# Kernel tuning notes

Hardware: AMD Instinct MI355X
Metric: run time of the kernel (lower is better)

Reference implementation:

```python
import jax, jax.numpy as jnp
import numpy as np

NH = 8  # n_heads
LN_EPS = 1e-5

def _ln(x, g, b):
    m = x.mean(-1, keepdims=True)
    v = ((x - m) ** 2).mean(-1, keepdims=True)
    return (x - m) / jnp.sqrt(v + LN_EPS) * g + b

def _l2norm(x):
    n = jnp.sqrt(jnp.sum(x * x, axis=-1, keepdims=True))
    return x / jnp.maximum(n, 1e-12)

def _block(h, inw, inb, outw, outb, g1, b1, g2, b2, w1, bb1, w2, bb2):
    B, T, D = h.shape
    hd = D // NH
    res = h
    hn = _ln(h, g1, b1)
    qkv = hn @ inw.T + inb
    q, k, v = jnp.split(qkv, 3, axis=-1)
    q = q.reshape(B, T, NH, hd)
    k = k.reshape(B, T, NH, hd)
    v = v.reshape(B, T, NH, hd)
    scores = jnp.einsum('bthd,bshd->bhts', q, k) / jnp.sqrt(jnp.asarray(hd, h.dtype))
    a = jax.nn.softmax(scores, axis=-1)
    o = jnp.einsum('bhts,bshd->bthd', a, v).reshape(B, T, D)
    h = res + o @ outw.T + outb
    f = _ln(h, g2, b2)
    f = jax.nn.gelu(f @ w1.T + bb1, approximate=False) @ w2.T + bb2
    return h + f

def setup_inputs() -> dict:
    B, T, IN, D, L, NS, NP = 8, 1024, 1024, 512, 4, 1024, 512
    key = jax.random.key(0)
    ks = jax.random.split(key, 24)
    gn = jax.random.normal
    u = jax.random.uniform(ks[1], (B, T, NS), dtype=jnp.float32, minval=1e-6, maxval=1.0 - 1e-6)
    gumbel = -jnp.log(-jnp.log(u))
    s = lambda fan: 1.0 / np.sqrt(fan)
    inp = {
        'x': gn(ks[0], (B, T, IN), dtype=jnp.float32),
        'gumbel': gumbel,
        'sym_w': gn(ks[2], (D, IN)) * s(IN),
        'sym_b': jnp.zeros((D,)),
        'codebook': gn(ks[3], (NS, D)) * 0.1,
        'pos_enc': gn(ks[4], (1, 2000, D)) * 0.02,
        'attn_in_w': gn(ks[5], (L, 3 * D, D)) * s(D),
        'attn_in_b': jnp.zeros((L, 3 * D)),
        'attn_out_w': gn(ks[6], (L, D, D)) * s(D),
        'attn_out_b': jnp.zeros((L, D)),
        'n1_g': jnp.ones((L, D)), 'n1_b': jnp.zeros((L, D)),
        'n2_g': jnp.ones((L, D)), 'n2_b': jnp.zeros((L, D)),
        'ffn_w1': gn(ks[7], (L, 4 * D, D)) * s(D),
        'ffn_b1': jnp.zeros((L, 4 * D)),
        'ffn_w2': gn(ks[8], (L, D, 4 * D)) * s(4 * D),
        'ffn_b2': jnp.zeros((L, D)),
        'q_w': gn(ks[9], (D, D)) * s(D),
        'q_b': jnp.zeros((D,)),
        'qln_g': jnp.ones((D,)), 'qln_b': jnp.zeros((D,)),
        'patterns': gn(ks[10], (NP, D)) * s(D),
        'epoch': 0,
        'total_epochs': 100,
    }
    return inp

def reference(x, gumbel, sym_w, sym_b, codebook, pos_enc,
              attn_in_w, attn_in_b, attn_out_w, attn_out_b,
              n1_g, n1_b, n2_g, n2_b, ffn_w1, ffn_b1, ffn_w2, ffn_b2,
              q_w, q_b, qln_g, qln_b, patterns, epoch, total_epochs):
    B, T, _ = x.shape
    # SymbolizationLayer (soft, gumbel-softmax with tau=0.5)
    hp = x @ sym_w.T + sym_b                               # [B,T,D]
    logits_s = _l2norm(hp) @ _l2norm(codebook).T / 0.5     # [B,T,NS]
    soft = jax.nn.softmax((logits_s + gumbel) / 0.5, axis=-1)
    h = soft @ codebook + pos_enc[:, :T, :]
    # transformer blocks
    for i in range(attn_in_w.shape[0]):
        h = _block(h, attn_in_w[i], attn_in_b[i], attn_out_w[i], attn_out_b[i],
                   n1_g[i], n1_b[i], n2_g[i], n2_b[i],
                   ffn_w1[i], ffn_b1[i], ffn_w2[i], ffn_b2[i])
    # VQPatternMatrix (eval mode: hard assignments, no EMA updates)
    Q = _l2norm(_ln(h @ q_w.T + q_b, qln_g, qln_b))
    temp = max(0.5, 1.0 - 0.5 * epoch / total_epochs)
    logits = Q @ _l2norm(patterns).T / temp                # [B,T,NP]
    hard_idx = jnp.argmax(logits, axis=-1)                 # [B,T]
    assign = jax.nn.one_hot(hard_idx, patterns.shape[0], dtype=logits.dtype)
    emb = jnp.take(patterns, hard_idx, axis=0)             # gather = one_hot @ patterns
    return (emb, assign, logits, h, hard_idx)
```

## Files before the change

### kernel.cpp

```cpp
#include <hip/hip_runtime.h>

#define DEV __device__ __forceinline__

typedef unsigned short u16;
typedef unsigned int u32;
typedef __attribute__((ext_vector_type(8))) _Float16 h8_t;
typedef __attribute__((ext_vector_type(4))) float f4_t;

constexpr int T_SEQ = 1024;
constexpr int DMODEL = 512;
constexpr int NPAT = 512;

enum {
  E_BIAS = 0,
  E_VQ = 5,
  E_RES = 6,
  E_POS = 8,
  E_GUM2 = 9,
  E_GELU2 = 10,
  E_QKV2 = 11
};

DEV float h2f(u16 h) { return (float)__builtin_bit_cast(_Float16, h); }
DEV void split2(float x, u16& h, u16& l) {
  _Float16 hh = (_Float16)x;
  float r = x - (float)hh;
  _Float16 ll = (_Float16)r;
  h = __builtin_bit_cast(u16, hh);
  l = __builtin_bit_cast(u16, ll);
}

DEV f4_t mfh(h8_t a, h8_t b, f4_t c) {
  return __builtin_amdgcn_mfma_f32_16x16x32_f16(a, b, c, 0, 0, 0);
}
DEV f4_t prod3(h8_t ah, h8_t al, h8_t bh, h8_t bl, f4_t c) {
  c = mfh(ah, bh, c);
  c = mfh(ah, bl, c);
  c = mfh(al, bh, c);
  return c;
}

typedef const __attribute__((address_space(1))) unsigned char* gas_t;
typedef __attribute__((address_space(3))) unsigned char* las_t;
DEV void gload16(const u16* g, u16* l) {
  __builtin_amdgcn_global_load_lds((gas_t)(const void*)g, (las_t)(void*)l, 16,
                                   0, 0);
}

template <int BM, int EPI>
__global__ __launch_bounds__(256, BM == 64 ? 3 : 2) void gemm_mf(
    const u16* __restrict__ Ah, const u16* __restrict__ Al,
    const u16* __restrict__ Bh, const u16* __restrict__ Bl,
    const float* __restrict__ bias, const float* __restrict__ res,
    float* __restrict__ Cf, u16* __restrict__ Ch, u16* __restrict__ Cl, int N,
    int KK, int lda, int ldb, int gx, const int* __restrict__ ep,
    const int* __restrict__ tot) {
  constexpr int MT = BM / 32;
  constexpr int CPP = BM / 16;
  __shared__ __align__(16) u16 AsH[2][BM][4][8], AsL[2][BM][4][8];
  __shared__ __align__(16) u16 BsH[2][128][4][8], BsL[2][128][4][8];
  const int tid = threadIdx.x;
  const int w = tid >> 6, lane = tid & 63;
  const int wy = w >> 1, wx = w & 1;
  const int lr = lane & 15, lg = lane >> 4;

  const int nwg = gridDim.x;
  const int bid = blockIdx.x;
  const int qq = nwg >> 3;
  const int wg = (bid & 7) * qq + (bid >> 3);
  const int by = wg / gx, bx = wg % gx;
  const int bm = by * BM, bn = bx * 128;

  const int rowl = lane >> 2, slot4 = lane & 3;

  auto STAGE = [&](int k0, int buf) {
#pragma unroll
    for (int it = 0; it < CPP / 2; ++it) {
      const int f = w + 4 * it;
      const int plane = f / CPP;
      const int ch = f % CPP;
      const int row = ch * 16 + rowl;
      const int kp = slot4 ^ ((row >> 1) & 3);
      const size_t g = (size_t)(bm + row) * lda + k0 + kp * 8;
      if (plane == 0)
        gload16(&Ah[g], &AsH[buf][0][0][0] + ch * 512);
      else
        gload16(&Al[g], &AsL[buf][0][0][0] + ch * 512);
    }
#pragma unroll
    for (int it = 0; it < 4; ++it) {
      const int f = w + 4 * it;
      const int plane = f >> 3;
      const int ch = f & 7;
      const int row = ch * 16 + rowl;
      const int kp = slot4 ^ ((row >> 1) & 3);
      const size_t g = (size_t)(bn + row) * ldb + k0 + kp * 8;
      if (plane == 0)
        gload16(&Bh[g], &BsH[buf][0][0][0] + ch * 512);
      else
        gload16(&Bl[g], &BsL[buf][0][0][0] + ch * 512);
    }
  };

  f4_t acc[MT][4];
#pragma unroll
  for (int mt = 0; mt < MT; ++mt)
#pragma unroll
    for (int nt = 0; nt < 4; ++nt) acc[mt][nt] = (f4_t){0.f, 0.f, 0.f, 0.f};

  const int nsteps = KK / 32;
  STAGE(0, 0);
  __syncthreads();
  for (int t = 0; t < nsteps; ++t) {
    const int cur = t & 1;
    if (t + 1 < nsteps) STAGE((t + 1) * 32, cur ^ 1);

    h8_t fah[MT], fal[MT], fbh[4], fbl[4];
#pragma unroll
    for (int mt = 0; mt < MT; ++mt) {
      int row = wy * (BM / 2) + mt * 16 + lr;
      int slot = lg ^ ((row >> 1) & 3);
      fah[mt] = *(const h8_t*)&AsH[cur][row][slot][0];
      fal[mt] = *(const h8_t*)&AsL[cur][row][slot][0];
    }
#pragma unroll
    for (int nt = 0; nt < 4; ++nt) {
      int col = wx * 64 + nt * 16 + lr;
      int slot = lg ^ ((col >> 1) & 3);
      fbh[nt] = *(const h8_t*)&BsH[cur][col][slot][0];
      fbl[nt] = *(const h8_t*)&BsL[cur][col][slot][0];
    }
#pragma unroll
    for (int mt = 0; mt < MT; ++mt)
#pragma unroll
      for (int nt = 0; nt < 4; ++nt)
        acc[mt][nt] = prod3(fah[mt], fal[mt], fbh[nt], fbl[nt], acc[mt][nt]);
    __syncthreads();
  }

  float bv[4];
  if constexpr (EPI == E_BIAS || EPI == E_RES || EPI == E_GELU2 ||
                EPI == E_QKV2) {
#pragma unroll
    for (int nt = 0; nt < 4; ++nt) bv[nt] = bias[bn + wx * 64 + nt * 16 + lr];
  }
  float invt = 1.0f;
  if constexpr (EPI == E_VQ) {
    float tt = 1.0f - 0.5f * (float)ep[0] / (float)tot[0];
    invt = 1.0f / fmaxf(0.5f, tt);
  }
#pragma unroll
  for (int mt = 0; mt < MT; ++mt)
#pragma unroll
    for (int nt = 0; nt < 4; ++nt) {
      const int c = bn + wx * 64 + nt * 16 + lr;
#pragma unroll
      for (int i = 0; i < 4; ++i) {
        const int m = bm + wy * (BM / 2) + mt * 16 + 4 * lg + i;
        const size_t idx = (size_t)m * N + c;
        float v = acc[mt][nt][i];
        if constexpr (EPI == E_BIAS) {
          Cf[idx] = v + bv[nt];
        } else if constexpr (EPI == E_VQ) {
          Cf[idx] = v * invt;
        } else if constexpr (EPI == E_RES) {
          Cf[idx] = v + bv[nt] + res[idx];
        } else if constexpr (EPI == E_POS) {
          Cf[idx] = v + res[(size_t)(m & 1023) * N + c];
        } else if constexpr (EPI == E_GUM2) {
          float t = 4.0f * v + 2.0f * res[idx];
          u16 h2, l2;
          split2(t, h2, l2);
          Ch[idx] = h2;
          Cl[idx] = l2;
        } else if constexpr (EPI == E_GELU2) {
          float t = v + bv[nt];
          float g = 0.5f * t * (1.0f + erff(t * 0.7071067811865476f));
          u16 h2, l2;
          split2(g, h2, l2);
          Ch[idx] = h2;
          Cl[idx] = l2;
        } else if constexpr (EPI == E_QKV2) {
          float t = v + bv[nt];
          u16 h2, l2;
          split2(t, h2, l2);
          size_t o;
          if (c < 512) {
            o = (size_t)m * 512 + c;
          } else if (c < 1024) {
            o = 4194304 + (size_t)m * 512 + (c - 512);
          } else {
            int cc = c - 1024, hh2 = cc >> 6, dd = cc & 63;
            int bb2 = m >> 10, tt2 = m & 1023;
            o = 8388608 +
                (((size_t)(bb2 * 8 + hh2) * 64 + dd) << 10) + tt2;
          }
          Ch[o] = h2;
          Cl[o] = l2;
        }
      }
    }
}

__global__ __launch_bounds__(256, 4) void flash_mfma(
    const u16* __restrict__ QKVh, const u16* __restrict__ QKVl,
    u16* __restrict__ Oh, u16* __restrict__ Ol) {
  __shared__ __align__(16) u16 KP[2][64][8][8];
  __shared__ __align__(16) u16 Vs[2][64][8][8];
  const int tid = threadIdx.x;
  const int w = tid >> 6, lane = tid & 63;
  const int lr = lane & 15, lg = lane >> 4;
  const int bid = blockIdx.x;
  const int b = bid & 7;
  const int slot_b = bid >> 3;
  const int hh = slot_b >> 4;
  const int qt = slot_b & 15;

  const u16* Qh = QKVh;
  const u16* Ql = QKVl;
  const u16* Kh = QKVh + 4194304;
  const u16* Kl = QKVl + 4194304;
  const u16* Vh = QKVh + 8388608;
  const u16* Vl = QKVl + 8388608;

  h8_t qf[2][2];
  {
    size_t g =
        ((size_t)(b * 1024 + qt * 64 + w * 16 + lr)) * 512 + hh * 64 + lg * 8;
    qf[0][0] = *(const h8_t*)&Qh[g];
    qf[0][1] = *(const h8_t*)&Ql[g];
    qf[1][0] = *(const h8_t*)&Qh[g + 32];
    qf[1][1] = *(const h8_t*)&Ql[g + 32];
  }

  f4_t oacc[4];
#pragma unroll
  for (int nt = 0; nt < 4; ++nt) oacc[nt] = (f4_t){0.f, 0.f, 0.f, 0.f};
  float mrun[4], lrun[4];
#pragma unroll
  for (int i = 0; i < 4; ++i) {
    mrun[i] = -__builtin_huge_valf();
    lrun[i] = 0.0f;
  }

  const int rowl8 = lane >> 3, slot8 = lane & 7;

  for (int kt = 0; kt < 16; ++kt) {
    __syncthreads();
#pragma unroll
    for (int it = 0; it < 4; ++it) {
      const int f = w + 4 * it;
      const int plane = f >> 3, ch = f & 7;
      const int row = ch * 8 + rowl8;
      const int kp = slot8 ^ (row & 7);
      const size_t gk =
          ((size_t)(b * 1024 + kt * 64 + row)) * 512 + hh * 64 + kp * 8;
      if (plane == 0)
        gload16(&Kh[gk], &KP[0][0][0][0] + ch * 512);
      else
        gload16(&Kl[gk], &KP[1][0][0][0] + ch * 512);
    }
#pragma unroll
    for (int it = 0; it < 4; ++it) {
      const int f = w + 4 * it;
      const int plane = f >> 3, ch = f & 7;
      const int row = ch * 8 + rowl8;
      const int kp = slot8 ^ (row & 7);
      const size_t gv =
          ((size_t)((b * 8 + hh) * 64 + row)) * 1024 + kt * 64 + kp * 8;
      if (plane == 0)
        gload16(&Vh[gv], &Vs[0][0][0][0] + ch * 512);
      else
        gload16(&Vl[gv], &Vs[1][0][0][0] + ch * 512);
    }
    __syncthreads();

    f4_t s[4];
#pragma unroll
    for (int nt = 0; nt < 4; ++nt) {
      s[nt] = (f4_t){0.f, 0.f, 0.f, 0.f};
      const int col = nt * 16 + lr;
#pragma unroll
      for (int ks = 0; ks < 2; ++ks) {
        int slt = (ks * 4 + lg) ^ (col & 7);
        h8_t kh = *(const h8_t*)&KP[0][col][slt][0];
        h8_t kl = *(const h8_t*)&KP[1][col][slt][0];
        s[nt] = prod3(qf[ks][0], qf[ks][1], kh, kl, s[nt]);
      }
    }

#pragma unroll
    for (int i = 0; i < 4; ++i) {
      float rm = -__builtin_huge_valf();
#pragma unroll
      for (int nt = 0; nt < 4; ++nt) {
        s[nt][i] *= 0.125f;
        rm = fmaxf(rm, s[nt][i]);
      }
      rm = fmaxf(rm, __shfl_xor(rm, 1));
      rm = fmaxf(rm, __shfl_xor(rm, 2));
      rm = fmaxf(rm, __shfl_xor(rm, 4));
      rm = fmaxf(rm, __shfl_xor(rm, 8));
      float mnew = fmaxf(mrun[i], rm);
      float alpha = __expf(mrun[i] - mnew);
      float rs = 0.0f;
#pragma unroll
      for (int nt = 0; nt < 4; ++nt) {
        float p = __expf(s[nt][i] - mnew);
        s[nt][i] = p;
        rs += p;
      }
      rs += __shfl_xor(rs, 1);
      rs += __shfl_xor(rs, 2);
      rs += __shfl_xor(rs, 4);
      rs += __shfl_xor(rs, 8);
      lrun[i] = lrun[i] * alpha + rs;
      mrun[i] = mnew;
#pragma unroll
      for (int nt = 0; nt < 4; ++nt) oacc[nt][i] *= alpha;
    }

    __syncthreads();

#pragma unroll
    for (int nt = 0; nt < 4; ++nt)
#pragma unroll
      for (int i = 0; i < 4; ++i) {
        int qrow = w * 16 + 4 * lg + i;
        int kv = nt * 16 + lr;
        int kp = kv >> 3, j = kv & 7;
        int slt = kp ^ (qrow & 7);
        u16 h2, l2;
        split2(s[nt][i], h2, l2);
        KP[0][qrow][slt][j] = h2;
        KP[1][qrow][slt][j] = l2;
      }

    h8_t pf[2][2];
#pragma unroll
    for (int ks = 0; ks < 2; ++ks) {
      int row = w * 16 + lr;
      int slt = (ks * 4 + lg) ^ (row & 7);
      pf[ks][0] = *(const h8_t*)&KP[0][row][slt][0];
      pf[ks][1] = *(const h8_t*)&KP[1][row][slt][0];
    }
#pragma unroll
    for (int ntd = 0; ntd < 4; ++ntd) {
      const int col = ntd * 16 + lr;
#pragma unroll
      for (int ks = 0; ks < 2; ++ks) {
        int slt = (ks * 4 + lg) ^ (col & 7);
        h8_t vh = *(const h8_t*)&Vs[0][col][slt][0];
        h8_t vl = *(const h8_t*)&Vs[1][col][slt][0];
        oacc[ntd] = prod3(pf[ks][0], pf[ks][1], vh, vl, oacc[ntd]);
      }
    }
  }

#pragma unroll
  for (int i = 0; i < 4; ++i) {
    float inv = 1.0f / lrun[i];
    int t = qt * 64 + w * 16 + 4 * lg + i;
#pragma unroll
    for (int ntd = 0; ntd < 4; ++ntd) {
      int d = hh * 64 + ntd * 16 + lr;
      size_t idx = ((size_t)(b * 1024 + t)) * 512 + d;
      u16 h2, l2;
      split2(oacc[ntd][i] * inv, h2, l2);
      Oh[idx] = h2;
      Ol[idx] = l2;
    }
  }
}

DEV float wave_sum(float v) {
#pragma unroll
  for (int off = 1; off < 64; off <<= 1) v += __shfl_xor(v, off);
  return v;
}

DEV void store8_split2(u16* H, u16* L, size_t base, const float* t) {
  u16 vh[8], vl[8];
#pragma unroll
  for (int j = 0; j < 8; ++j) split2(t[j], vh[j], vl[j]);
  *(ushort4*)&H[base] = make_ushort4(vh[0], vh[1], vh[2], vh[3]);
  *(ushort4*)&H[base + 4] = make_ushort4(vh[4], vh[5], vh[6], vh[7]);
  *(ushort4*)&L[base] = make_ushort4(vl[0], vl[1], vl[2], vl[3]);
  *(ushort4*)&L[base + 4] = make_ushort4(vl[4], vl[5], vl[6], vl[7]);
}

__global__ __launch_bounds__(256) void ln_split2(const float* __restrict__ x,
                                                 const float* __restrict__ g,
                                                 const float* __restrict__ b,
                                                 u16* __restrict__ yh,
                                                 u16* __restrict__ yl) {
  const int row = blockIdx.x * 4 + (threadIdx.x >> 6);
  const int lane = threadIdx.x & 63;
  const float* xr = x + (size_t)row * DMODEL;
  float v[8];
  *(float4*)&v[0] = *(const float4*)(xr + lane * 8);
  *(float4*)&v[4] = *(const float4*)(xr + lane * 8 + 4);
  float s = 0.0f;
#pragma unroll
  for (int j = 0; j < 8; ++j) s += v[j];
  s = wave_sum(s);
  float mean = s * (1.0f / 512.0f);
  float s2 = 0.0f;
#pragma unroll
  for (int j = 0; j < 8; ++j) {
    float d = v[j] - mean;
    s2 += d * d;
  }
  s2 = wave_sum(s2);
  float rstd = 1.0f / sqrtf(s2 * (1.0f / 512.0f) + 1e-5f);
  float gg[8], bv[8];
  *(float4*)&gg[0] = *(const float4*)(g + lane * 8);
  *(float4*)&gg[4] = *(const float4*)(g + lane * 8 + 4);
  *(float4*)&bv[0] = *(const float4*)(b + lane * 8);
  *(float4*)&bv[4] = *(const float4*)(b + lane * 8 + 4);
  float t[8];
#pragma unroll
  for (int j = 0; j < 8; ++j) t[j] = (v[j] - mean) * rstd * gg[j] + bv[j];
  store8_split2(yh, yl, (size_t)row * DMODEL + lane * 8, t);
}

__global__ __launch_bounds__(256) void ln_l2_split2(
    const float* __restrict__ x, const float* __restrict__ g,
    const float* __restrict__ b, u16* __restrict__ yh, u16* __restrict__ yl) {
  const int row = blockIdx.x * 4 + (threadIdx.x >> 6);
  const int lane = threadIdx.x & 63;
  const float* xr = x + (size_t)row * DMODEL;
  float v[8];
  *(float4*)&v[0] = *(const float4*)(xr + lane * 8);
  *(float4*)&v[4] = *(const float4*)(xr + lane * 8 + 4);
  float s = 0.0f;
#pragma unroll
  for (int j = 0; j < 8; ++j) s += v[j];
  s = wave_sum(s);
  float mean = s * (1.0f / 512.0f);
  float s2 = 0.0f;
#pragma unroll
  for (int j = 0; j < 8; ++j) {
    float d = v[j] - mean;
    s2 += d * d;
  }
  s2 = wave_sum(s2);
  float rstd = 1.0f / sqrtf(s2 * (1.0f / 512.0f) + 1e-5f);
  float gg[8], bv[8];
  *(float4*)&gg[0] = *(const float4*)(g + lane * 8);
  *(float4*)&gg[4] = *(const float4*)(g + lane * 8 + 4);
  *(float4*)&bv[0] = *(const float4*)(b + lane * 8);
  *(float4*)&bv[4] = *(const float4*)(b + lane * 8 + 4);
  float t[8];
#pragma unroll
  for (int j = 0; j < 8; ++j) t[j] = (v[j] - mean) * rstd * gg[j] + bv[j];
  float n2 = 0.0f;
#pragma unroll
  for (int j = 0; j < 8; ++j) n2 += t[j] * t[j];
  n2 = wave_sum(n2);
  float den = fmaxf(sqrtf(n2), 1e-12f);
#pragma unroll
  for (int j = 0; j < 8; ++j) t[j] /= den;
  store8_split2(yh, yl, (size_t)row * DMODEL + lane * 8, t);
}

__global__ __launch_bounds__(256) void l2_split2(const float* __restrict__ x,
                                                 u16* __restrict__ yh,
                                                 u16* __restrict__ yl) {
  const int row = blockIdx.x * 4 + (threadIdx.x >> 6);
  const int lane = threadIdx.x & 63;
  const float* xr = x + (size_t)row * DMODEL;
  float v[8];
  *(float4*)&v[0] = *(const float4*)(xr + lane * 8);
  *(float4*)&v[4] = *(const float4*)(xr + lane * 8 + 4);
  float n2 = 0.0f;
#pragma unroll
  for (int j = 0; j < 8; ++j) n2 += v[j] * v[j];
  n2 = wave_sum(n2);
  float den = fmaxf(sqrtf(n2), 1e-12f);
#pragma unroll
  for (int j = 0; j < 8; ++j) v[j] /= den;
  store8_split2(yh, yl, (size_t)row * DMODEL + lane * 8, v);
}

__global__ __launch_bounds__(256) void softmax2(u16* __restrict__ H,
                                                u16* __restrict__ L) {
  const int row = blockIdx.x;
  const int tid = threadIdx.x;
  const size_t base = (size_t)row * 1024 + tid * 4;
  ushort4 qh = *(const ushort4*)&H[base];
  ushort4 ql = *(const ushort4*)&L[base];
  float v0 = h2f(qh.x) + h2f(ql.x);
  float v1 = h2f(qh.y) + h2f(ql.y);
  float v2 = h2f(qh.z) + h2f(ql.z);
  float v3 = h2f(qh.w) + h2f(ql.w);
  float mx = fmaxf(fmaxf(v0, v1), fmaxf(v2, v3));
#pragma unroll
  for (int off = 1; off < 64; off <<= 1) mx = fmaxf(mx, __shfl_xor(mx, off));
  __shared__ float red[4];
  const int wv = tid >> 6;
  if ((tid & 63) == 0) red[wv] = mx;
  __syncthreads();
  mx = fmaxf(fmaxf(red[0], red[1]), fmaxf(red[2], red[3]));
  float e0 = __expf(v0 - mx), e1 = __expf(v1 - mx), e2 = __expf(v2 - mx),
        e3 = __expf(v3 - mx);
  float s = e0 + e1 + e2 + e3;
#pragma unroll
  for (int off = 1; off < 64; off <<= 1) s += __shfl_xor(s, off);
  __syncthreads();
  if ((tid & 63) == 0) red[wv] = s;
  __syncthreads();
  s = red[0] + red[1] + red[2] + red[3];
  float inv = 1.0f / s;
  u16 ah[4], al[4];
  split2(e0 * inv, ah[0], al[0]);
  split2(e1 * inv, ah[1], al[1]);
  split2(e2 * inv, ah[2], al[2]);
  split2(e3 * inv, ah[3], al[3]);
  *(ushort4*)&H[base] = make_ushort4(ah[0], ah[1], ah[2], ah[3]);
  *(ushort4*)&L[base] = make_ushort4(al[0], al[1], al[2], al[3]);
}

__global__ __launch_bounds__(256) void split2_k(const float* __restrict__ src,
                                                u16* __restrict__ H,
                                                u16* __restrict__ L, int n4) {
  for (int e = blockIdx.x * 256 + threadIdx.x; e < n4; e += gridDim.x * 256) {
    float4 v = *(const float4*)(src + (size_t)e * 4);
    u16 ah[4], al[4];
    split2(v.x, ah[0], al[0]);
    split2(v.y, ah[1], al[1]);
    split2(v.z, ah[2], al[2]);
    split2(v.w, ah[3], al[3]);
    *(ushort4*)&H[(size_t)e * 4] = make_ushort4(ah[0], ah[1], ah[2], ah[3]);
    *(ushort4*)&L[(size_t)e * 4] = make_ushort4(al[0], al[1], al[2], al[3]);
  }
}

__global__ __launch_bounds__(256) void tsplit_cb(const float* __restrict__ cb,
                                                 u16* __restrict__ th,
                                                 u16* __restrict__ tl) {
  const int c = blockIdx.x;
  const int t = threadIdx.x;
  u16 ah[4], al[4];
#pragma unroll
  for (int j = 0; j < 4; ++j) {
    float v = cb[(size_t)(4 * t + j) * 512 + c];
    split2(v, ah[j], al[j]);
  }
  const size_t base = (size_t)c * 1024 + 4 * t;
  *(ushort4*)&th[base] = make_ushort4(ah[0], ah[1], ah[2], ah[3]);
  *(ushort4*)&tl[base] = make_ushort4(al[0], al[1], al[2], al[3]);
}

__global__ __launch_bounds__(256) void vq_finalize(
    const float* __restrict__ logits, const float* __restrict__ patterns,
    float* __restrict__ emb, float* __restrict__ assign,
    float* __restrict__ idxf) {
  const int row = blockIdx.x * 4 + (threadIdx.x >> 6);
  const int lane = threadIdx.x & 63;
  const float* lr = logits + (size_t)row * NPAT;
  float best = -__builtin_huge_valf();
  int bi = 0;
#pragma unroll
  for (int jj = 0; jj < 8; ++jj) {
    int j = lane + jj * 64;
    float v = lr[j];
    if (v > best) {
      best = v;
      bi = j;
    }
  }
#pragma unroll
  for (int off = 1; off < 64; off <<= 1) {
    float ob = __shfl_xor(best, off);
    int oi = __shfl_xor(bi, off);
    if (ob > best || (ob == best && oi < bi)) {
      best = ob;
      bi = oi;
    }
  }
  const float* pr = patterns + (size_t)bi * DMODEL;
#pragma unroll
  for (int g = 0; g < 2; ++g) {
    int c = lane * 8 + g * 4;
    float4 pv = *(const float4*)(pr + c);
    *(float4*)(emb + (size_t)row * DMODEL + c) = pv;
    float4 av;
    av.x = (c + 0 == bi) ? 1.0f : 0.0f;
    av.y = (c + 1 == bi) ? 1.0f : 0.0f;
    av.z = (c + 2 == bi) ? 1.0f : 0.0f;
    av.w = (c + 3 == bi) ? 1.0f : 0.0f;
    *(float4*)(assign + (size_t)row * NPAT + c) = av;
  }
  if (lane == 0) idxf[row] = (float)bi;
}

extern "C" void kernel_launch(void* const* d_in, const int* in_sizes, int n_in,
                              void* d_out, int out_size, void* d_ws,
                              size_t ws_size, hipStream_t stream) {
  (void)in_sizes;
  (void)n_in;
  (void)out_size;
  (void)ws_size;
  const float* x = (const float*)d_in[0];
  const float* gumbel = (const float*)d_in[1];
  const float* sym_w = (const float*)d_in[2];
  const float* sym_b = (const float*)d_in[3];
  const float* codebook = (const float*)d_in[4];
  const float* pos_enc = (const float*)d_in[5];
  const float* attn_in_w = (const float*)d_in[6];
  const float* attn_in_b = (const float*)d_in[7];
  const float* attn_out_w = (const float*)d_in[8];
  const float* attn_out_b = (const float*)d_in[9];
  const float* n1_g = (const float*)d_in[10];
  const float* n1_b = (const float*)d_in[11];
  const float* n2_g = (const float*)d_in[12];
  const float* n2_b = (const float*)d_in[13];
  const float* ffn_w1 = (const float*)d_in[14];
  const float* ffn_b1 = (const float*)d_in[15];
  const float* ffn_w2 = (const float*)d_in[16];
  const float* ffn_b2 = (const float*)d_in[17];
  const float* q_w = (const float*)d_in[18];
  const float* q_b = (const float*)d_in[19];
  const float* qln_g = (const float*)d_in[20];
  const float* qln_b = (const float*)d_in[21];
  const float* patterns = (const float*)d_in[22];
  const int* epoch = (const int*)d_in[23];
  const int* tot = (const int*)d_in[24];

  float* out = (float*)d_out;
  float* emb = out;
  float* assign = out + 4194304;
  float* logits = out + 8388608;
  float* h = out + 12582912;
  float* idxf = out + 16777216;

  float* ws_f = (float*)d_ws;
  u16* a16 = (u16*)ws_f;
  float* bF = ws_f + 18874368;
  u16* b16 = (u16*)bF;
  u16 *hnH = b16, *hnL = b16 + 4194304;
  float* wF = ws_f + 25165824;
  u16* w16 = (u16*)wF;

  u16 *xH = a16, *xL = a16 + 8388608;
  split2_k<<<2048, 256, 0, stream>>>(x, xH, xL, 2097152);
  split2_k<<<512, 256, 0, stream>>>(sym_w, w16, w16 + 524288, 131072);
  gemm_mf<64, E_BIAS><<<512, 256, 0, stream>>>(
      xH, xL, w16, w16 + 524288, sym_b, nullptr, bF, nullptr, nullptr, 512,
      1024, 1024, 1024, 4, nullptr, nullptr);
  l2_split2<<<256, 256, 0, stream>>>(codebook, w16, w16 + 524288);
  u16 *hpH = a16, *hpL = a16 + 4194304;
  l2_split2<<<2048, 256, 0, stream>>>(bF, hpH, hpL);
  u16 *sH = a16 + 12582912, *sL = a16 + 20971520;
  gemm_mf<64, E_GUM2><<<1024, 256, 0, stream>>>(
      hpH, hpL, w16, w16 + 524288, nullptr, gumbel, nullptr, sH, sL, 1024, 512,
      512, 512, 8, nullptr, nullptr);
  softmax2<<<8192, 256, 0, stream>>>(sH, sL);
  tsplit_cb<<<512, 256, 0, stream>>>(codebook, w16, w16 + 524288);
  gemm_mf<64, E_POS><<<512, 256, 0, stream>>>(
      sH, sL, w16, w16 + 524288, nullptr, pos_enc, h, nullptr, nullptr, 512,
      1024, 1024, 1024, 4, nullptr, nullptr);

  u16 *qkvH = a16, *qkvL = a16 + 12582912;
  u16* w1p = a16 + 33554432;
  u16* w2p = b16 + 8388608;
  u16 *pH = a16, *pL = a16 + 16777216;

  for (int l = 0; l < 4; ++l) {
    const float* inw = attn_in_w + (size_t)l * 1536 * 512;
    const float* inb = attn_in_b + (size_t)l * 1536;
    const float* outw = attn_out_w + (size_t)l * 512 * 512;
    const float* outb = attn_out_b + (size_t)l * 512;
    const float* w1 = ffn_w1 + (size_t)l * 2048 * 512;
    const float* b1 = ffn_b1 + (size_t)l * 2048;
    const float* w2 = ffn_w2 + (size_t)l * 512 * 2048;
    const float* b2 = ffn_b2 + (size_t)l * 512;

    ln_split2<<<2048, 256, 0, stream>>>(h, n1_g + l * 512, n1_b + l * 512,
                                        hnH, hnL);
    split2_k<<<1024, 256, 0, stream>>>(inw, w16, w16 + 786432, 196608);
    gemm_mf<128, E_QKV2><<<768, 256, 0, stream>>>(
        hnH, hnL, w16, w16 + 786432, inb, nullptr, nullptr, qkvH, qkvL, 1536,
        512, 512, 512, 12, nullptr, nullptr);
    flash_mfma<<<1024, 256, 0, stream>>>(qkvH, qkvL, hnH, hnL);
    split2_k<<<256, 256, 0, stream>>>(outw, w16, w16 + 262144, 65536);
    gemm_mf<64, E_RES><<<512, 256, 0, stream>>>(
        hnH, hnL, w16, w16 + 262144, outb, h, h, nullptr, nullptr, 512, 512,
        512, 512, 4, nullptr, nullptr);
    ln_split2<<<2048, 256, 0, stream>>>(h, n2_g + l * 512, n2_b + l * 512,
                                        hnH, hnL);
    split2_k<<<1024, 256, 0, stream>>>(w1, w1p, w1p + 1048576, 262144);
    split2_k<<<1024, 256, 0, stream>>>(w2, w2p, w2p + 1048576, 262144);
    gemm_mf<128, E_GELU2><<<1024, 256, 0, stream>>>(
        hnH, hnL, w1p, w1p + 1048576, b1, nullptr, nullptr, pH, pL, 2048, 512,
        512, 512, 16, nullptr, nullptr);
    gemm_mf<64, E_RES><<<512, 256, 0, stream>>>(
        pH, pL, w2p, w2p + 1048576, b2, h, h, nullptr, nullptr, 512, 2048,
        2048, 2048, 4, nullptr, nullptr);
  }

  u16 *hsH = a16, *hsL = a16 + 4194304;
  u16 *QpH = a16 + 8388608, *QpL = a16 + 12582912;
  split2_k<<<1024, 256, 0, stream>>>(h, hsH, hsL, 1048576);
  split2_k<<<256, 256, 0, stream>>>(q_w, w16, w16 + 262144, 65536);
  gemm_mf<64, E_BIAS><<<512, 256, 0, stream>>>(
      hsH, hsL, w16, w16 + 262144, q_b, nullptr, bF, nullptr, nullptr, 512,
      512, 512, 512, 4, nullptr, nullptr);
  ln_l2_split2<<<2048, 256, 0, stream>>>(bF, qln_g, qln_b, QpH, QpL);
  l2_split2<<<128, 256, 0, stream>>>(patterns, w16 + 524288, w16 + 786432);
  gemm_mf<64, E_VQ><<<512, 256, 0, stream>>>(
      QpH, QpL, w16 + 524288, w16 + 786432, nullptr, nullptr, logits, nullptr,
      nullptr, 512, 512, 512, 512, 4, epoch, tot);
  vq_finalize<<<2048, 256, 0, stream>>>(logits, patterns, emb, assign, idxf);
}
```

Before: 1.618 ms.

## Double query tile per flash-attention block to reuse K/V tiles

Each flash-attention block now handles 128 query rows instead of 64, with each wave processing two 16-row query sub-tiles against the same K and V fragments loaded into shared memory. This halves K/V global loads and LDS fragment reads per query row and halves the grid size. In exchange it raises register pressure (launch bounds lowered to 3 blocks per CU), grows shared memory for the P staging buffer, and gives fewer blocks to spread across CUs.

Result: slower. 1.751 ms (+8.2%).

```diff
diff --git a/kernel.cpp b/kernel.cpp
--- a/kernel.cpp
+++ b/kernel.cpp
@@ -202,10 +202,10 @@
     }
 }
 
-__global__ __launch_bounds__(256, 4) void flash_mfma(
+__global__ __launch_bounds__(256, 3) void flash_mfma(
     const u16* __restrict__ QKVh, const u16* __restrict__ QKVl,
     u16* __restrict__ Oh, u16* __restrict__ Ol) {
-  __shared__ __align__(16) u16 KP[2][64][8][8];
+  __shared__ __align__(16) u16 KP[2][128][8][8];
   __shared__ __align__(16) u16 Vs[2][64][8][8];
   const int tid = threadIdx.x;
   const int w = tid >> 6, lane = tid & 63;
@@ -213,8 +213,8 @@
   const int bid = blockIdx.x;
   const int b = bid & 7;
   const int slot_b = bid >> 3;
-  const int hh = slot_b >> 4;
-  const int qt = slot_b & 15;
+  const int hh = slot_b >> 3;
+  const int qt = slot_b & 7;
 
   const u16* Qh = QKVh;
   const u16* Ql = QKVl;
@@ -223,25 +223,30 @@
   const u16* Vh = QKVh + 8388608;
   const u16* Vl = QKVl + 8388608;
 
-  h8_t qf[2][2];
-  {
-    size_t g =
-        ((size_t)(b * 1024 + qt * 64 + w * 16 + lr)) * 512 + hh * 64 + lg * 8;
-    qf[0][0] = *(const h8_t*)&Qh[g];
-    qf[0][1] = *(const h8_t*)&Ql[g];
-    qf[1][0] = *(const h8_t*)&Qh[g + 32];
-    qf[1][1] = *(const h8_t*)&Ql[g + 32];
-  }
-
-  f4_t oacc[4];
-#pragma unroll
-  for (int nt = 0; nt < 4; ++nt) oacc[nt] = (f4_t){0.f, 0.f, 0.f, 0.f};
-  float mrun[4], lrun[4];
-#pragma unroll
-  for (int i = 0; i < 4; ++i) {
-    mrun[i] = -__builtin_huge_valf();
-    lrun[i] = 0.0f;
-  }
+  h8_t qf[2][2][2];
+#pragma unroll
+  for (int mq = 0; mq < 2; ++mq) {
+    size_t g = ((size_t)(b * 1024 + qt * 128 + w * 32 + mq * 16 + lr)) * 512 +
+               hh * 64 + lg * 8;
+    qf[mq][0][0] = *(const h8_t*)&Qh[g];
+    qf[mq][0][1] = *(const h8_t*)&Ql[g];
+    qf[mq][1][0] = *(const h8_t*)&Qh[g + 32];
+    qf[mq][1][1] = *(const h8_t*)&Ql[g + 32];
+  }
+
+  f4_t oacc[2][4];
+#pragma unroll
+  for (int mq = 0; mq < 2; ++mq)
+#pragma unroll
+    for (int nt = 0; nt < 4; ++nt) oacc[mq][nt] = (f4_t){0.f, 0.f, 0.f, 0.f};
+  float mrun[2][4], lrun[2][4];
+#pragma unroll
+  for (int mq = 0; mq < 2; ++mq)
+#pragma unroll
+    for (int i = 0; i < 4; ++i) {
+      mrun[mq][i] = -__builtin_huge_valf();
+      lrun[mq][i] = 0.0f;
+    }
 
   const int rowl8 = lane >> 3, slot8 = lane & 7;
 
@@ -275,75 +280,86 @@
     }
     __syncthreads();
 
-    f4_t s[4];
+    f4_t s[2][4];
+#pragma unroll
+    for (int mq = 0; mq < 2; ++mq)
+#pragma unroll
+      for (int nt = 0; nt < 4; ++nt) s[mq][nt] = (f4_t){0.f, 0.f, 0.f, 0.f};
 #pragma unroll
     for (int nt = 0; nt < 4; ++nt) {
-      s[nt] = (f4_t){0.f, 0.f, 0.f, 0.f};
       const int col = nt * 16 + lr;
 #pragma unroll
       for (int ks = 0; ks < 2; ++ks) {
         int slt = (ks * 4 + lg) ^ (col & 7);
         h8_t kh = *(const h8_t*)&KP[0][col][slt][0];
         h8_t kl = *(const h8_t*)&KP[1][col][slt][0];
-        s[nt] = prod3(qf[ks][0], qf[ks][1], kh, kl, s[nt]);
+#pragma unroll
+        for (int mq = 0; mq < 2; ++mq)
+          s[mq][nt] = prod3(qf[mq][ks][0], qf[mq][ks][1], kh, kl, s[mq][nt]);
       }
     }
 
 #pragma unroll
-    for (int i = 0; i < 4; ++i) {
-      float rm = -__builtin_huge_valf();
-#pragma unroll
-      for (int nt = 0; nt < 4; ++nt) {
-        s[nt][i] *= 0.125f;
-        rm = fmaxf(rm, s[nt][i]);
+    for (int mq = 0; mq < 2; ++mq)
+#pragma unroll
+      for (int i = 0; i < 4; ++i) {
+        float rm = -__builtin_huge_valf();
+#pragma unroll
+        for (int nt = 0; nt < 4; ++nt) {
+          s[mq][nt][i] *= 0.125f;
+          rm = fmaxf(rm, s[mq][nt][i]);
+        }
+        rm = fmaxf(rm, __shfl_xor(rm, 1));
+        rm = fmaxf(rm, __shfl_xor(rm, 2));
+        rm = fmaxf(rm, __shfl_xor(rm, 4));
+        rm = fmaxf(rm, __shfl_xor(rm, 8));
+        float mnew = fmaxf(mrun[mq][i], rm);
+        float alpha = __expf(mrun[mq][i] - mnew);
+        float rs = 0.0f;
+#pragma unroll
+        for (int nt = 0; nt < 4; ++nt) {
+          float p = __expf(s[mq][nt][i] - mnew);
+          s[mq][nt][i] = p;
+          rs += p;
+        }
+        rs += __shfl_xor(rs, 1);
+        rs += __shfl_xor(rs, 2);
+        rs += __shfl_xor(rs, 4);
+        rs += __shfl_xor(rs, 8);
+        lrun[mq][i] = lrun[mq][i] * alpha + rs;
+        mrun[mq][i] = mnew;
+#pragma unroll
+        for (int nt = 0; nt < 4; ++nt) oacc[mq][nt][i] *= alpha;
       }
-      rm = fmaxf(rm, __shfl_xor(rm, 1));
-      rm = fmaxf(rm, __shfl_xor(rm, 2));
-      rm = fmaxf(rm, __shfl_xor(rm, 4));
-      rm = fmaxf(rm, __shfl_xor(rm, 8));
-      float mnew = fmaxf(mrun[i], rm);
-      float alpha = __expf(mrun[i] - mnew);
-      float rs = 0.0f;
-#pragma unroll
-      for (int nt = 0; nt < 4; ++nt) {
-        float p = __expf(s[nt][i] - mnew);
-        s[nt][i] = p;
-        rs += p;
+
+    __syncthreads();
+
+#pragma unroll
+    for (int mq = 0; mq < 2; ++mq)
+#pragma unroll
+      for (int nt = 0; nt < 4; ++nt)
+#pragma unroll
+        for (int i = 0; i < 4; ++i) {
+          int qrow = w * 32 + mq * 16 + 4 * lg + i;
+          int kv = nt * 16 + lr;
+          int kp = kv >> 3, j = kv & 7;
+          int slt = kp ^ (qrow & 7);
+          u16 h2, l2;
+          split2(s[mq][nt][i], h2, l2);
+          KP[0][qrow][slt][j] = h2;
+          KP[1][qrow][slt][j] = l2;
+        }
+
+    h8_t pf[2][2][2];
+#pragma unroll
+    for (int mq = 0; mq < 2; ++mq)
+#pragma unroll
+      for (int ks = 0; ks < 2; ++ks) {
+        int row = w * 32 + mq * 16 + lr;
+        int slt = (ks * 4 + lg) ^ (row & 7);
+        pf[mq][ks][0] = *(const h8_t*)&KP[0][row][slt][0];
+        pf[mq][ks][1] = *(const h8_t*)&KP[1][row][slt][0];
       }
-      rs += __shfl_xor(rs, 1);
-      rs += __shfl_xor(rs, 2);
-      rs += __shfl_xor(rs, 4);
-      rs += __shfl_xor(rs, 8);
-      lrun[i] = lrun[i] * alpha + rs;
-      mrun[i] = mnew;
-#pragma unroll
-      for (int nt = 0; nt < 4; ++nt) oacc[nt][i] *= alpha;
-    }
-
-    __syncthreads();
-
-#pragma unroll
-    for (int nt = 0; nt < 4; ++nt)
-#pragma unroll
-      for (int i = 0; i < 4; ++i) {
-        int qrow = w * 16 + 4 * lg + i;
-        int kv = nt * 16 + lr;
-        int kp = kv >> 3, j = kv & 7;
-        int slt = kp ^ (qrow & 7);
-        u16 h2, l2;
-        split2(s[nt][i], h2, l2);
-        KP[0][qrow][slt][j] = h2;
-        KP[1][qrow][slt][j] = l2;
-      }
-
-    h8_t pf[2][2];
-#pragma unroll
-    for (int ks = 0; ks < 2; ++ks) {
-      int row = w * 16 + lr;
-      int slt = (ks * 4 + lg) ^ (row & 7);
-      pf[ks][0] = *(const h8_t*)&KP[0][row][slt][0];
-      pf[ks][1] = *(const h8_t*)&KP[1][row][slt][0];
-    }
 #pragma unroll
     for (int ntd = 0; ntd < 4; ++ntd) {
       const int col = ntd * 16 + lr;
@@ -352,25 +368,30 @@
         int slt = (ks * 4 + lg) ^ (col & 7);
         h8_t vh = *(const h8_t*)&Vs[0][col][slt][0];
         h8_t vl = *(const h8_t*)&Vs[1][col][slt][0];
-        oacc[ntd] = prod3(pf[ks][0], pf[ks][1], vh, vl, oacc[ntd]);
+#pragma unroll
+        for (int mq = 0; mq < 2; ++mq)
+          oacc[mq][ntd] =
+              prod3(pf[mq][ks][0], pf[mq][ks][1], vh, vl, oacc[mq][ntd]);
       }
     }
   }
 
 #pragma unroll
-  for (int i = 0; i < 4; ++i) {
-    float inv = 1.0f / lrun[i];
-    int t = qt * 64 + w * 16 + 4 * lg + i;
-#pragma unroll
-    for (int ntd = 0; ntd < 4; ++ntd) {
-      int d = hh * 64 + ntd * 16 + lr;
-      size_t idx = ((size_t)(b * 1024 + t)) * 512 + d;
-      u16 h2, l2;
-      split2(oacc[ntd][i] * inv, h2, l2);
-      Oh[idx] = h2;
-      Ol[idx] = l2;
-    }
-  }
+  for (int mq = 0; mq < 2; ++mq)
+#pragma unroll
+    for (int i = 0; i < 4; ++i) {
+      float inv = 1.0f / lrun[mq][i];
+      int t = qt * 128 + w * 32 + mq * 16 + 4 * lg + i;
+#pragma unroll
+      for (int ntd = 0; ntd < 4; ++ntd) {
+        int d = hh * 64 + ntd * 16 + lr;
+        size_t idx = ((size_t)(b * 1024 + t)) * 512 + d;
+        u16 h2, l2;
+        split2(oacc[mq][ntd][i] * inv, h2, l2);
+        Oh[idx] = h2;
+        Ol[idx] = l2;
+      }
+    }
 }
 
 DEV float wave_sum(float v) {
@@ -683,7 +704,7 @@
     gemm_mf<128, E_QKV2><<<768, 256, 0, stream>>>(
         hnH, hnL, w16, w16 + 786432, inb, nullptr, nullptr, qkvH, qkvL, 1536,
         512, 512, 512, 12, nullptr, nullptr);
-    flash_mfma<<<1024, 256, 0, stream>>>(qkvH, qkvL, hnH, hnL);
+    flash_mfma<<<512, 256, 0, stream>>>(qkvH, qkvL, hnH, hnL);
     split2_k<<<256, 256, 0, stream>>>(outw, w16, w16 + 262144, 65536);
     gemm_mf<64, E_RES><<<512, 256, 0, stream>>>(
         hnH, hnL, w16, w16 + 262144, outb, h, h, nullptr, nullptr, 512, 512,
```
